# Kernel optimization log

Hardware: AMD Instinct MI355X
Metric: run time of the kernel (lower is better)

The kernel has to match this reference:

```python
import jax, jax.numpy as jnp
import numpy as np

B = 1; C = 96; NH = 4; HD = 24; WIN = 3; LL = 27; SR = 8
Dd, Hh, Ww = 16, 40, 40
N = Dd * Hh * Ww
pH, pW, pD = Hh // SR, Ww // SR, Dd // SR
PL = pH * pW * pD
T = 4096


def _build_mask():
    p = WIN // 2
    m = np.zeros((Dd + 2 * p, Hh + 2 * p, Ww + 2 * p), bool)
    m[p:Dd + p, p:Hh + p, p:Ww + p] = True
    pats = np.stack([m[dz:dz + Dd, dy:dy + Hh, dx:dx + Ww]
                     for dz in range(WIN) for dy in range(WIN) for dx in range(WIN)], axis=-1)
    return jnp.asarray(~pats.reshape(N, LL))  # True where padded (masked)

MASK = _build_mask()


def _layernorm(x, w, b, eps=1e-5):
    mu = jnp.mean(x, axis=-1, keepdims=True)
    var = jnp.var(x, axis=-1, keepdims=True)
    return (x - mu) / jnp.sqrt(var + eps) * w + b


def _l2(x, eps=1e-12):
    n = jnp.sqrt(jnp.sum(x * x, axis=-1, keepdims=True))
    return x / jnp.maximum(n, eps)


def _unfold3d(x):
    # x: (B,C,D,H,W) -> (B,C,N,27), kernel order (kd,kh,kw) as torch unfold(2).unfold(3).unfold(4)
    p = WIN // 2
    xp = jnp.pad(x, ((0, 0), (0, 0), (p, p), (p, p), (p, p)))
    pats = [xp[:, :, dz:dz + Dd, dy:dy + Hh, dx:dx + Ww]
            for dz in range(WIN) for dy in range(WIN) for dx in range(WIN)]
    return jnp.stack(pats, axis=-1).reshape(x.shape[0], C, N, LL)


def _conv3(x, w):
    return jax.lax.conv_general_dilated(x, w, (1, 1, 1), 'SAME',
                                        dimension_numbers=('NCDHW', 'OIDHW', 'NCDHW'))


def _bn(x, p, eps=1e-5):
    sh = (1, C, 1, 1, 1)
    return (x - p[2].reshape(sh)) / jnp.sqrt(p[3].reshape(sh) + eps) * p[0].reshape(sh) + p[1].reshape(sh)


def _lrelu(x):
    return jnp.where(x >= 0, x, 0.01 * x)


def _resblock(x, w1, p1, w2, p2):
    h = _lrelu(_bn(_conv3(x, w1), p1))
    h = _bn(_conv3(h, w2), p2)
    return _lrelu(h + x)


def _forward(x, relative_pos_index, relative_coords_table, seq_length_scale,
             norm_w, norm_b, gamma, w_qkvv, temperature, temperature2, query_embedding,
             rel_bias_local, learnable_tokens, learnable_bias, sr_w, sr_b,
             epa_norm_w, epa_norm_b, w_kv, cpb1_w, cpb1_b, cpb2_w, cpb2_b,
             out1_w, out1_b, out2_w, out2_b,
             c51a_w, c51a_bn, c51b_w, c51b_bn, c52a_w, c52a_bn, c52b_w, c52b_bn,
             conv8_w, conv8_b):
    Bq = x.shape[0]
    # flatten (D,H,W) -> N tokens; pos_embed=True adds 1.0 (faithful to `x + True`)
    xt = x.reshape(Bq, C, N).transpose(0, 2, 1) + 1.0
    xn = _layernorm(xt, norm_w, norm_b)
    qkvv = (xn @ w_qkvv.T).reshape(Bq, N, 4, NH, HD).transpose(2, 0, 3, 1, 4)
    q, k, v_ca, v_sa = qkvv[0], qkvv[1], qkvv[2], qkvv[3]  # (B,NH,N,HD)
    qn = _l2(q)
    qs = (qn + query_embedding) * (jax.nn.softplus(temperature) * seq_length_scale)
    k_img = k.transpose(0, 1, 3, 2).reshape(Bq, C, Dd, Hh, Ww)
    v_img = v_sa.transpose(0, 1, 3, 2).reshape(Bq, C, Dd, Hh, Ww)
    k_loc = _unfold3d(k_img).reshape(Bq, NH, HD, N, LL).transpose(0, 1, 3, 2, 4)  # (B,NH,N,HD,LL)
    v_loc = _unfold3d(v_img).reshape(Bq, NH, HD, N, LL).transpose(0, 1, 3, 2, 4)
    a_loc = jnp.einsum('bhnd,bhndk->bhnk', qs, k_loc) + rel_bias_local[:, None, :]
    a_loc = jnp.where(MASK[None, None], -jnp.inf, a_loc)
    # pooled branch (note faithful (H,W,D) reshape as in source)
    xp = xn.transpose(0, 2, 1).reshape(Bq, C, Hh, Ww, Dd)
    xp = jax.nn.gelu(jnp.einsum('oc,bcxyz->boxyz', sr_w, xp)
                     + sr_b[None, :, None, None, None], approximate=False)
    xp = xp.reshape(Bq, C, pH, SR, pW, SR, pD, SR).mean(axis=(3, 5, 7))  # adaptive avg pool
    xp = xp.reshape(Bq, C, PL).transpose(0, 2, 1)
    xp = _layernorm(xp, epa_norm_w, epa_norm_b)
    kv = (xp @ w_kv.T).reshape(Bq, PL, 2 * NH, HD).transpose(0, 2, 1, 3)
    k_pool, v_pool = kv[:, :NH], kv[:, NH:]
    tab = jax.nn.relu(relative_coords_table @ cpb1_w.T + cpb1_b) @ cpb2_w.T + cpb2_b  # (T,NH)
    pool_bias = jnp.take(tab.T, relative_pos_index.reshape(-1), axis=1).reshape(NH, N, PL)
    a_pool = jnp.einsum('bhnd,bhpd->bhnp', qs, _l2(k_pool)) + pool_bias[None]
    attn = jax.nn.softmax(jnp.concatenate([a_loc, a_pool], axis=-1), axis=-1)
    a_loc, a_pool = attn[..., :LL], attn[..., LL:]
    a_loc = jnp.einsum('bhnd,hdk->bhnk', qn, learnable_tokens) + learnable_bias[None] + a_loc
    x_loc = jnp.einsum('bhnk,bhndk->bhnd', a_loc, v_loc)
    x_pool = jnp.einsum('bhnp,bhpd->bhnd', a_pool, v_pool)
    x_sa = (x_loc + x_pool).transpose(0, 2, 1, 3).reshape(Bq, N, C)
    # channel attention branch
    qt = _l2(q.transpose(0, 1, 3, 2))
    kt = _l2(k.transpose(0, 1, 3, 2))
    vt = v_ca.transpose(0, 1, 3, 2)
    a_ca = jax.nn.softmax(jnp.einsum('bhdn,bhen->bhde', qt, kt) * temperature2, axis=-1)
    x_ca = jnp.einsum('bhde,bhen->bhdn', a_ca, vt).transpose(0, 3, 1, 2).reshape(Bq, N, C)
    epa = jnp.concatenate([x_sa @ out1_w.T + out1_b, x_ca @ out2_w.T + out2_b], axis=-1)
    ax = xt + gamma * epa
    skip = ax.reshape(Bq, Hh, Ww, Dd, C).transpose(0, 4, 1, 2, 3)  # (B,C,H,W,D)
    h = _resblock(skip, c51a_w, c51a_bn, c51b_w, c51b_bn)
    h = _resblock(h, c52a_w, c52a_bn, c52b_w, c52b_bn)
    return skip + jnp.einsum('oc,bcxyz->boxyz', conv8_w, h) + conv8_b[None, :, None, None, None]


def setup_inputs():
    key = jax.random.key(0)
    ks = iter(jax.random.split(key, 64))
    r = lambda shape, s=0.02: jax.random.normal(next(ks), shape, jnp.float32) * s
    d = {}
    d['x'] = jax.random.normal(next(ks), (B, C, Dd, Hh, Ww), jnp.float32)
    d['relative_pos_index'] = jax.random.randint(next(ks), (N * PL,), 0, T, jnp.int32)
    d['relative_coords_table'] = jax.random.normal(next(ks), (T, 3), jnp.float32)
    d['seq_length_scale'] = jnp.ones((1,), jnp.float32)
    d['norm_w'] = 1.0 + r((C,)); d['norm_b'] = r((C,))
    d['gamma'] = jnp.full((C,), 0.01, jnp.float32)
    d['w_qkvv'] = r((4 * C, C))
    d['temperature'] = jnp.full((NH, 1, 1), float(np.log(np.exp(1 / 0.24) - 1)), jnp.float32)
    d['temperature2'] = jnp.ones((NH, 1, 1), jnp.float32)
    d['query_embedding'] = r((NH, 1, HD))
    d['rel_bias_local'] = r((NH, LL), 0.0004)
    d['learnable_tokens'] = r((NH, HD, LL))
    d['learnable_bias'] = jnp.zeros((NH, 1, LL), jnp.float32)
    d['sr_w'] = r((C, C)); d['sr_b'] = r((C,))
    d['epa_norm_w'] = 1.0 + r((C,)); d['epa_norm_b'] = r((C,))
    d['w_kv'] = r((2 * C, C))
    d['cpb1_w'] = r((512, 3)); d['cpb1_b'] = r((512,))
    d['cpb2_w'] = r((NH, 512)); d['cpb2_b'] = r((NH,))
    d['out1_w'] = r((C // 2, C)); d['out1_b'] = r((C // 2,))
    d['out2_w'] = r((C // 2, C)); d['out2_b'] = r((C // 2,))
    bn = lambda: jnp.stack([1.0 + r((C,)), r((C,)), jnp.zeros((C,), jnp.float32), jnp.ones((C,), jnp.float32)])
    d['c51a_w'] = r((C, C, 3, 3, 3)); d['c51a_bn'] = bn()
    d['c51b_w'] = r((C, C, 3, 3, 3)); d['c51b_bn'] = bn()
    d['c52a_w'] = r((C, C, 3, 3, 3)); d['c52a_bn'] = bn()
    d['c52b_w'] = r((C, C, 3, 3, 3)); d['c52b_bn'] = bn()
    d['conv8_w'] = r((C, C)); d['conv8_b'] = r((C,))
    return d


def reference(x, relative_pos_index, relative_coords_table, seq_length_scale,
              norm_w, norm_b, gamma, w_qkvv, temperature, temperature2, query_embedding,
              rel_bias_local, learnable_tokens, learnable_bias, sr_w, sr_b,
              epa_norm_w, epa_norm_b, w_kv, cpb1_w, cpb1_b, cpb2_w, cpb2_b,
              out1_w, out1_b, out2_w, out2_b,
              c51a_w, c51a_bn, c51b_w, c51b_bn, c52a_w, c52a_bn, c52b_w, c52b_bn,
              conv8_w, conv8_b):
    return _forward(x, relative_pos_index, relative_coords_table, seq_length_scale,
                    norm_w, norm_b, gamma, w_qkvv, temperature, temperature2, query_embedding,
                    rel_bias_local, learnable_tokens, learnable_bias, sr_w, sr_b,
                    epa_norm_w, epa_norm_b, w_kv, cpb1_w, cpb1_b, cpb2_w, cpb2_b,
                    out1_w, out1_b, out2_w, out2_b,
                    c51a_w, c51a_bn, c51b_w, c51b_bn, c52a_w, c52a_bn, c52b_w, c52b_bn,
                    conv8_w, conv8_b)
```

## Files before the change

### kernel.cpp

```cpp
#include <hip/hip_runtime.h>
#include <hip/hip_bf16.h>

#define NN 25600
#define CC 96
#define NHh 4
#define HDd 24
#define SSLOT 2457600
#define WP 269568

typedef unsigned short ushort_t;
typedef float f32x4 __attribute__((ext_vector_type(4)));
typedef short s16x8 __attribute__((ext_vector_type(8)));
typedef _Float16 f16;
typedef f16 h2v __attribute__((ext_vector_type(2)));

__device__ __forceinline__ float LD(const void* p, int i){
  return ((const float*)p)[i];
}
__device__ __forceinline__ float b2f(ushort_t u){ return __uint_as_float(((unsigned)u)<<16); }
__device__ __forceinline__ ushort_t f2b(float f){
  unsigned u = __float_as_uint(f);
  unsigned r = (u + 0x7fffu + ((u>>16)&1u))>>16;
  return (ushort_t)r;
}
__device__ __forceinline__ ushort_t f2h(float f){
  f16 hv = (f16)f;
  return *reinterpret_cast<ushort_t*>(&hv);
}
__device__ __forceinline__ float fdot2(h2v a, h2v b, float c){
#if __has_builtin(__builtin_amdgcn_fdot2)
  return __builtin_amdgcn_fdot2(a, b, c, false);
#else
  return c + (float)a[0]*(float)b[0] + (float)a[1]*(float)b[1];
#endif
}
__device__ __forceinline__ void gl_lds16(const void* g, const void* l){
  __builtin_amdgcn_global_load_lds(
      (const __attribute__((address_space(1))) unsigned*)g,
      (__attribute__((address_space(3))) unsigned*)l, 16, 0, 0);
}

#define NEGINF (-3.0e38f)

__global__ __launch_bounds__(256) void k_ln2(
    const void* __restrict__ x, const void* __restrict__ nw,
    const void* __restrict__ nb, ushort_t* __restrict__ XNH){
  __shared__ float reds[4][64], redss[4][64];
  __shared__ ushort_t OUT[64][100];
  int tid = threadIdx.x, nl = tid&63, cg = tid>>6;
  int n = blockIdx.x*64 + nl;
  float v[24]; float s=0.f, ss=0.f;
  #pragma unroll
  for(int i=0;i<24;i++){
    float t = LD(x, (cg*24+i)*NN + n) + 1.0f;
    v[i]=t; s+=t; ss+=t*t;
  }
  reds[cg][nl]=s; redss[cg][nl]=ss;
  __syncthreads();
  float S  = reds[0][nl]+reds[1][nl]+reds[2][nl]+reds[3][nl];
  float SS = redss[0][nl]+redss[1][nl]+redss[2][nl]+redss[3][nl];
  float mu = S*(1.0f/CC);
  float inv = rsqrtf(SS*(1.0f/CC) - mu*mu + 1e-5f);
  #pragma unroll
  for(int i=0;i<24;i++){
    int c = cg*24+i;
    OUT[nl][c] = f2b((v[i]-mu)*inv*LD(nw,c) + LD(nb,c));
  }
  __syncthreads();
  for(int f=tid; f<3072; f+=256){
    int r = f/48, dp = f%48;
    unsigned pk = (unsigned)OUT[r][dp*2] | ((unsigned)OUT[r][dp*2+1]<<16);
    *reinterpret_cast<unsigned*>(XNH + (size_t)(blockIdx.x*64+r)*96 + dp*2) = pk;
  }
}

__global__ void k_prepall(
    const void* w0, const void* w1, const void* w2, const void* w3,
    const void* wq, const void* wsr, const void* w8,
    const void* o1w, const void* o1b, const void* o2w, const void* o2b,
    const void* b0, const void* b1, const void* b2, const void* b3,
    const void* ltok,
    ushort_t* __restrict__ WB2, ushort_t* __restrict__ WQH,
    ushort_t* __restrict__ WSH, ushort_t* __restrict__ W8H,
    ushort_t* __restrict__ WE, float* __restrict__ EB,
    float* __restrict__ BNS, ushort_t* __restrict__ LTOKT,
    float* __restrict__ ZB){
  int e = blockIdx.x*256 + threadIdx.x;
  if(e < 4*WP){
    int t = e/WP, r = e%WP;
    int tap = r/9984, r2 = r%9984, o = r2/104, p = r2%104;
    const void* w = (t==0)? w0 : (t==1)? w1 : (t==2)? w2 : w3;
    WB2[e] = (p<96)? f2b(LD(w, (o*96+p)*27 + tap)) : (ushort_t)0;
  }
  if(e < 36864) WQH[e] = f2b(LD(wq,e));
  if(e < 9216){ WSH[e] = f2b(LD(wsr,e)); W8H[e] = f2b(LD(w8,e)); }
  if(e < 96*192){
    int o = e/192, c2 = e%192;
    float v = 0.f;
    if(o < 48 && c2 < 96)        v = LD(o1w, o*96 + c2);
    else if(o >= 48 && c2 >= 96) v = LD(o2w, (o-48)*96 + (c2-96));
    WE[e] = f2b(v);
    if(c2 == 0) EB[o] = (o<48)? LD(o1b,o) : LD(o2b,o-48);
  }
  if(e < 384){
    int t = e/96, o = e%96;
    const void* bn = (t==0)? b0 : (t==1)? b1 : (t==2)? b2 : b3;
    float g=LD(bn,o), b=LD(bn,96+o), mu=LD(bn,192+o), var=LD(bn,288+o);
    float s = g*rsqrtf(var+1e-5f);
    BNS[t*192+o] = s;
    BNS[t*192+96+o] = b - mu*s;
  }
  if(e < 4096){
    int h = e/1024, r = e%1024, kk = r/32, d = r%32;
    float v = (d<24 && kk<27)? LD(ltok, (h*24+d)*27 + kk) : 0.f;
    LTOKT[e] = f2b(v);
  }
  if(e < 8) ZB[e] = 0.f;
}

__global__ __launch_bounds__(256) void k_rpit2(const int* __restrict__ rpi,
                                               int* __restrict__ rpiT){
  __shared__ int T[50][65];
  int n0 = blockIdx.x*64;
  int tid = threadIdx.x;
  for(int f=tid; f<3200; f+=256){
    int nl = f/50, p = f%50;
    T[p][nl] = rpi[n0*50 + f];
  }
  __syncthreads();
  for(int f=tid; f<3200; f+=256){
    int p = f>>6, nl = f&63;
    rpiT[(size_t)p*NN + n0 + nl] = T[p][nl];
  }
}

__global__ __launch_bounds__(256,2) void k_qkvsr(
    const ushort_t* __restrict__ XNH, const ushort_t* __restrict__ WQH,
    const ushort_t* __restrict__ WSH, const void* __restrict__ srb,
    float* __restrict__ out, ushort_t* __restrict__ KH,
    ushort_t* __restrict__ VH, float* __restrict__ XP2){
  int tid=threadIdx.x, w=tid>>6, lane=tid&63, lan=lane&15, grp=lane>>4;
  int n = blockIdx.x*64 + w*16 + lan;
  const ushort_t* bp = XNH + n*96;
  if(blockIdx.y < 2){
    int ybase = blockIdx.y*192;
    f32x4 acc[12];
    #pragma unroll
    for(int mt=0;mt<12;mt++) acc[mt] = (f32x4)(0.f);
    #pragma unroll
    for(int s=0;s<3;s++){
      s16x8 b = *reinterpret_cast<const s16x8*>(bp + s*32 + grp*8);
      #pragma unroll
      for(int mt=0;mt<12;mt++){
        s16x8 a = *reinterpret_cast<const s16x8*>(WQH + (ybase+mt*16+lan)*96 + s*32 + grp*8);
        acc[mt] = __builtin_amdgcn_mfma_f32_16x16x32_bf16(a, b, acc[mt], 0,0,0);
      }
    }
    #pragma unroll
    for(int mt=0;mt<12;mt++){
      int o0 = ybase + mt*16 + grp*4;
      int sl = o0/96, rr = o0%96, h = rr/24, dd = rr%24;
      f32x4 v = acc[mt];
      if(sl == 3){
        ushort4 pk = { f2h(v[0]), f2h(v[1]), f2h(v[2]), f2h(v[3]) };
        *reinterpret_cast<ushort4*>(VH + ((size_t)h*NN+n)*24 + dd) = pk;
      } else {
        *reinterpret_cast<float4*>(out + sl*SSLOT + ((size_t)h*NN+n)*24 + dd) =
            (float4){v[0],v[1],v[2],v[3]};
        if(sl == 1){
          ushort4 pk = { f2h(v[0]), f2h(v[1]), f2h(v[2]), f2h(v[3]) };
          *reinterpret_cast<ushort4*>(KH + ((size_t)h*NN+n)*24 + dd) = pk;
        }
      }
    }
  } else {
    f32x4 acc[6];
    #pragma unroll
    for(int mt=0;mt<6;mt++) acc[mt] = (f32x4)(0.f);
    #pragma unroll
    for(int s=0;s<3;s++){
      s16x8 b = *reinterpret_cast<const s16x8*>(bp + s*32 + grp*8);
      #pragma unroll
      for(int mt=0;mt<6;mt++){
        s16x8 a = *reinterpret_cast<const s16x8*>(WSH + (mt*16+lan)*96 + s*32 + grp*8);
        acc[mt] = __builtin_amdgcn_mfma_f32_16x16x32_bf16(a, b, acc[mt], 0,0,0);
      }
    }
    #pragma unroll
    for(int mt=0;mt<6;mt++){
      #pragma unroll
      for(int r=0;r<4;r++){
        int o = mt*16 + grp*4 + r;
        float y = acc[mt][r] + LD(srb,o);
        y = 0.5f*y*(1.0f + erff(y*0.70710678118f));
        XP2[o*NN+n] = y;
      }
    }
  }
}

__global__ void k_qs2(const float* __restrict__ Q, const void* __restrict__ temp,
                      const void* __restrict__ sls, const void* __restrict__ qe,
                      ushort_t* __restrict__ QNH, float* __restrict__ QS){
  int id = blockIdx.x*256 + threadIdx.x;
  if(id >= NHh*NN) return;
  int h = id/NN, n = id%NN;
  const float* qr = Q + ((size_t)h*NN+n)*24;
  float qv[24]; float ss=0.f;
  #pragma unroll
  for(int d=0;d<24;d++){ qv[d]=qr[d]; ss+=qv[d]*qv[d]; }
  float inv = 1.0f/fmaxf(sqrtf(ss), 1e-12f);
  float t = LD(temp,h);
  float sp = log1pf(expf(t)) * LD(sls,0);
  ushort_t* qo = QNH + ((size_t)h*NN+n)*32;
  float* qs = QS + ((size_t)h*NN+n)*24;
  #pragma unroll
  for(int d=0;d<24;d+=2){
    float q0 = qv[d]*inv, q1 = qv[d+1]*inv;
    unsigned pk = (unsigned)f2b(q0) | ((unsigned)f2b(q1)<<16);
    *reinterpret_cast<unsigned*>(qo + d) = pk;
    qs[d]   = (q0 + LD(qe, h*24+d))*sp;
    qs[d+1] = (q1 + LD(qe, h*24+d+1))*sp;
  }
  *reinterpret_cast<unsigned*>(qo+24)=0; *reinterpret_cast<unsigned*>(qo+26)=0;
  *reinterpret_cast<unsigned*>(qo+28)=0; *reinterpret_cast<unsigned*>(qo+30)=0;
}

__global__ __launch_bounds__(256) void k_ltm(
    const ushort_t* __restrict__ QNH, const ushort_t* __restrict__ LTOKT,
    const void* __restrict__ lbias, ushort_t* __restrict__ LTH){
  int tid=threadIdx.x, h=tid>>6, lane=tid&63, lan=lane&15, grp=lane>>4;
  int n0 = blockIdx.x*64;
  f32x4 acc[4][2];
  #pragma unroll
  for(int j=0;j<4;j++)
    #pragma unroll
    for(int t=0;t<2;t++) acc[j][t] = (f32x4)(0.f);
  #pragma unroll
  for(int j=0;j<4;j++){
    int n = n0 + j*16 + lan;
    s16x8 b = *reinterpret_cast<const s16x8*>(QNH + ((size_t)h*NN+n)*32 + grp*8);
    #pragma unroll
    for(int t=0;t<2;t++){
      s16x8 a = *reinterpret_cast<const s16x8*>(LTOKT + h*1024 + (t*16+lan)*32 + grp*8);
      acc[j][t] = __builtin_amdgcn_mfma_f32_16x16x32_bf16(a, b, acc[j][t], 0,0,0);
    }
  }
  #pragma unroll
  for(int j=0;j<4;j++){
    int n = n0 + j*16 + lan;
    #pragma unroll
    for(int t=0;t<2;t++){
      int k0 = t*16 + grp*4;
      if(k0 < 28){
        ushort4 pk;
        ushort_t* pp = reinterpret_cast<ushort_t*>(&pk);
        #pragma unroll
        for(int r=0;r<4;r++){
          int k = k0+r;
          float v = acc[j][t][r] + ((k<27)? LD(lbias, h*27+k) : 0.f);
          pp[r] = f2h(v);
        }
        *reinterpret_cast<ushort4*>(LTH + ((size_t)h*NN+n)*28 + k0) = pk;
      }
    }
  }
}

__global__ void k_pool(const float* __restrict__ XP2, float* __restrict__ pooled){
  int bb = blockIdx.x;
  int c = bb % CC, p = bb / CC;
  int ph = p/10, pw = (p%10)/2, pd = p%2;
  float s = 0.f;
  for(int t=threadIdx.x; t<512; t+=64){
    int i=t>>6, j=(t>>3)&7, k=t&7;
    int m = (ph*8+i)*640 + (pw*8+j)*16 + (pd*8+k);
    s += XP2[c*NN+m];
  }
  #pragma unroll
  for(int off=32;off;off>>=1) s += __shfl_down(s, off);
  if(threadIdx.x==0) pooled[p*CC+c] = s*(1.0f/512.0f);
}

__global__ void k_lnkv(const float* __restrict__ pooled, const void* __restrict__ ew,
                       const void* __restrict__ eb, const void* __restrict__ wkv,
                       float* __restrict__ KP, ushort_t* __restrict__ VPH){
  __shared__ float row[96], lnr[96], st[2];
  int p = blockIdx.x, t = threadIdx.x;
  if(t<96) row[t] = pooled[p*96+t];
  __syncthreads();
  if(t==0){
    float s=0.f, ss=0.f;
    for(int c=0;c<96;c++){ float v=row[c]; s+=v; ss+=v*v; }
    float mu=s*(1.0f/96.0f);
    float var=ss*(1.0f/96.0f)-mu*mu;
    st[0]=mu; st[1]=rsqrtf(var+1e-5f);
  }
  __syncthreads();
  if(t<96) lnr[t] = (row[t]-st[0])*st[1]*LD(ew,t) + LD(eb,t);
  __syncthreads();
  if(t<192){
    float a=0.f;
    for(int c=0;c<96;c++) a += LD(wkv, t*96+c)*lnr[c];
    int g=t/24, d=t%24;
    if(g<4) KP[(g*50+p)*24+d]=a;
    else    VPH[((g-4)*50+p)*24+d] = f2h(a);
  }
}

__global__ void k_kpn(const float* __restrict__ KP, ushort_t* __restrict__ KPNH){
  int t = threadIdx.x;
  if(t>=200) return;
  const float* r = KP + t*24;
  float ss=0.f;
  #pragma unroll
  for(int d=0;d<24;d++) ss += r[d]*r[d];
  float inv = 1.0f/fmaxf(sqrtf(ss),1e-12f);
  #pragma unroll
  for(int d=0;d<24;d++) KPNH[t*24+d] = f2h(r[d]*inv);
}

__global__ void k_tab(const void* __restrict__ rct, const void* __restrict__ w1,
                      const void* __restrict__ b1, const void* __restrict__ w2,
                      const void* __restrict__ b2, float* __restrict__ TAB){
  __shared__ float red[32];
  int tt = blockIdx.x, j = threadIdx.x;
  float r0=LD(rct,tt*3), r1=LD(rct,tt*3+1), r2=LD(rct,tt*3+2);
  float hj = r0*LD(w1,j*3) + r1*LD(w1,j*3+1) + r2*LD(w1,j*3+2) + LD(b1,j);
  hj = fmaxf(hj, 0.f);
  int lane=j&63, wid=j>>6;
  for(int h=0;h<4;h++){
    float v = hj*LD(w2, h*512+j);
    #pragma unroll
    for(int off=32;off;off>>=1) v += __shfl_down(v, off);
    if(lane==0) red[wid*4+h]=v;
  }
  __syncthreads();
  if(j<4){
    float s=0.f;
    for(int w=0;w<8;w++) s += red[w*4+j];
    TAB[tt*4+j] = s + LD(b2,j);
  }
}

__global__ __launch_bounds__(512) void k_attn6(
    const float* __restrict__ QS, const ushort_t* __restrict__ KH,
    const ushort_t* __restrict__ VH,
    const ushort_t* __restrict__ KPNH, const ushort_t* __restrict__ VPH,
    const float* __restrict__ TAB, const int* __restrict__ rpiT,
    const void* __restrict__ rbl, const ushort_t* __restrict__ LTH,
    ushort_t* __restrict__ XH)
{
  __shared__ ushort_t KVH[2][600*26];
  int tile = blockIdx.x, h = blockIdx.y;
  int g = tile/25, sp = tile%25, hg = sp/5, wg = sp%5;
  int tid = threadIdx.x;
  int role = tid>>8, q = tid & 255;
  int wq = q>>6, l = q&63;
  int hy = l>>3, wx = l&7;
  int d0 = g*4 + wq;
  int h0 = hg*8+hy, w0 = wg*8+wx;
  int n = d0*1600 + h0*40 + w0;

  const ushort_t* KHh = KH + (size_t)h*NN*24;
  const ushort_t* VHh = VH + (size_t)h*NN*24;
  for(int f=tid; f<3600; f+=512){
    int t = f/1800, rem = f%1800, row = rem/3, qq = rem%3;
    int dr = row/100, yr = (row%100)/10, xr = row%10;
    int zc = min(max(g*4+dr-1,0),15), yc = min(max(hg*8+yr-1,0),39), xc = min(max(wg*8+xr-1,0),39);
    const ushort_t* src = (t? VHh : KHh) + (size_t)(zc*1600+yc*40+xc)*24 + qq*8;
    const unsigned* s32 = reinterpret_cast<const unsigned*>(src);
    unsigned a0=s32[0], a1=s32[1], a2=s32[2], a3=s32[3];
    unsigned* d32 = reinterpret_cast<unsigned*>(&KVH[t][row*26 + qq*8]);
    d32[0]=a0; d32[1]=a1; d32[2]=a2; d32[3]=a3;
  }

  h2v qp[12];
  {
    const float* qsp = QS + ((size_t)h*NN+n)*24;
    #pragma unroll
    for(int d=0; d<24; d+=4){
      float4 a = *reinterpret_cast<const float4*>(qsp+d);
      qp[d/2]   = (h2v){ (f16)a.x, (f16)a.y };
      qp[d/2+1] = (h2v){ (f16)a.z, (f16)a.w };
    }
  }
  __syncthreads();

  float m_r, s_r;
  h2v accA[12], accT[12];
  #pragma unroll
  for(int j=0;j<12;j++){ accA[j]=(h2v){(f16)0.f,(f16)0.f}; accT[j]=(h2v){(f16)0.f,(f16)0.f}; }

  const h2v* kph = reinterpret_cast<const h2v*>(KPNH) + (size_t)h*50*12;
  const h2v* vph = reinterpret_cast<const h2v*>(VPH)  + (size_t)h*50*12;

  if(role==0){
    float av[39]; unsigned okm=0;
    #pragma unroll
    for(int k=0;k<27;k++){
      int kz=k/9, ky=(k%9)/3, kx=k%3;
      bool ok = (unsigned)(d0+kz-1)<16u && (unsigned)(h0+ky-1)<40u && (unsigned)(w0+kx-1)<40u;
      float sc = NEGINF;
      if(ok){
        okm |= 1u<<k;
        const h2v* kr = reinterpret_cast<const h2v*>(
            &KVH[0][((wq+kz)*100 + (hy+ky)*10 + (wx+kx))*26]);
        sc = LD(rbl, h*27+k);
        #pragma unroll
        for(int j=0;j<12;j++) sc = fdot2(kr[j], qp[j], sc);
      }
      av[k]=sc;
    }
    #pragma unroll
    for(int p=0;p<12;p++){
      float sc = TAB[rpiT[(size_t)p*NN+n]*4 + h];
      const h2v* kr = kph + p*12;
      #pragma unroll
      for(int j=0;j<12;j++) sc = fdot2(kr[j], qp[j], sc);
      av[27+p]=sc;
    }
    float m = av[0];
    #pragma unroll
    for(int k=1;k<39;k++) m = fmaxf(m, av[k]);
    const f16* ltp = reinterpret_cast<const f16*>(LTH) + ((size_t)h*NN+n)*28;
    float s = 0.f;
    #pragma unroll
    for(int k=0;k<27;k++){
      if(okm>>k & 1u){
        int kz=k/9, ky=(k%9)/3, kx=k%3;
        float e = __expf(av[k]-m);
        s += e;
        float ltv = (float)ltp[k];
        h2v we = { (f16)e, (f16)e };
        h2v wt = { (f16)ltv, (f16)ltv };
        const h2v* vr = reinterpret_cast<const h2v*>(
            &KVH[1][((wq+kz)*100 + (hy+ky)*10 + (wx+kx))*26]);
        #pragma unroll
        for(int j=0;j<12;j++){
          accA[j] = vr[j]*we + accA[j];
          accT[j] = vr[j]*wt + accT[j];
        }
      }
    }
    #pragma unroll
    for(int p=0;p<12;p++){
      float e = __expf(av[27+p]-m);
      s += e;
      h2v we = { (f16)e, (f16)e };
      const h2v* vr = vph + p*12;
      #pragma unroll
      for(int j=0;j<12;j++) accA[j] = vr[j]*we + accA[j];
    }
    m_r = m; s_r = s;
  } else {
    float av[38];
    #pragma unroll
    for(int p=0;p<38;p++){
      int pp = p+12;
      float sc = TAB[rpiT[(size_t)pp*NN+n]*4 + h];
      const h2v* kr = kph + pp*12;
      #pragma unroll
      for(int j=0;j<12;j++) sc = fdot2(kr[j], qp[j], sc);
      av[p]=sc;
    }
    float m = av[0];
    #pragma unroll
    for(int p=1;p<38;p++) m = fmaxf(m, av[p]);
    float s = 0.f;
    #pragma unroll
    for(int p=0;p<38;p++){
      float e = __expf(av[p]-m);
      s += e;
      h2v we = { (f16)e, (f16)e };
      const h2v* vr = vph + (p+12)*12;
      #pragma unroll
      for(int j=0;j<12;j++) accA[j] = vr[j]*we + accA[j];
    }
    m_r = m; s_r = s;
  }
  __syncthreads();

  float* PP = (float*)&KVH[0][0];
  if(role==1){
    PP[q*15+0] = m_r;
    PP[q*15+1] = s_r;
    #pragma unroll
    for(int j=0;j<12;j++){
      h2v a = accA[j];
      PP[q*15+2+j] = __uint_as_float(*reinterpret_cast<unsigned*>(&a));
    }
  }
  __syncthreads();

  float* TRF = (float*)&KVH[0][0] + 4096;
  if(role==0){
    float mp = PP[q*15+0], sp2 = PP[q*15+1];
    float m = fmaxf(m_r, mp);
    float a = __expf(m_r - m), b = __expf(mp - m);
    float inv = 1.0f/(a*s_r + b*sp2);
    #pragma unroll
    for(int j=0;j<12;j++){
      unsigned pb = __float_as_uint(PP[q*15+2+j]);
      h2v ap = *reinterpret_cast<h2v*>(&pb);
      float v0 = (a*(float)accA[j][0] + b*(float)ap[0])*inv + (float)accT[j][0];
      float v1 = (a*(float)accA[j][1] + b*(float)ap[1])*inv + (float)accT[j][1];
      TRF[q*25 + 2*j]   = v0;
      TRF[q*25 + 2*j+1] = v1;
    }
  }
  __syncthreads();

  for(int f=tid; f<3072; f+=512){
    int q2 = f/12, dp = f%12;
    int w2 = q2>>6, l2 = q2&63;
    int n2 = (g*4+w2)*1600 + (hg*8+(l2>>3))*40 + (wg*8+(l2&7));
    float v0 = TRF[q2*25+dp*2], v1 = TRF[q2*25+dp*2+1];
    unsigned pk = (unsigned)f2b(v0) | ((unsigned)f2b(v1)<<16);
    *reinterpret_cast<unsigned*>(XH + (size_t)n2*192 + h*24 + dp*2) = pk;
  }
}

__global__ void k_cascore2(const float* __restrict__ Q, const float* __restrict__ K,
                           float* __restrict__ PAR){
  __shared__ float red[4][26];
  int hd = blockIdx.x, h = hd/24, d = hd%24;
  int n0 = blockIdx.y*3200;
  float acc[24]; float qss=0.f, kss=0.f;
  #pragma unroll
  for(int e=0;e<24;e++) acc[e]=0.f;
  for(int i=threadIdx.x; i<3200; i+=256){
    int n = n0 + i;
    const float4* kr4 = reinterpret_cast<const float4*>(K + ((size_t)h*NN+n)*24);
    float4 k0=kr4[0], k1=kr4[1], k2=kr4[2], k3=kr4[3], k4=kr4[4], k5=kr4[5];
    float qv = Q[((size_t)h*NN+n)*24+d];
    qss += qv*qv;
    float kd = LD(K, ((size_t)h*NN+n)*24+d);
    kss += kd*kd;
    acc[0]+=qv*k0.x; acc[1]+=qv*k0.y; acc[2]+=qv*k0.z; acc[3]+=qv*k0.w;
    acc[4]+=qv*k1.x; acc[5]+=qv*k1.y; acc[6]+=qv*k1.z; acc[7]+=qv*k1.w;
    acc[8]+=qv*k2.x; acc[9]+=qv*k2.y; acc[10]+=qv*k2.z; acc[11]+=qv*k2.w;
    acc[12]+=qv*k3.x; acc[13]+=qv*k3.y; acc[14]+=qv*k3.z; acc[15]+=qv*k3.w;
    acc[16]+=qv*k4.x; acc[17]+=qv*k4.y; acc[18]+=qv*k4.z; acc[19]+=qv*k4.w;
    acc[20]+=qv*k5.x; acc[21]+=qv*k5.y; acc[22]+=qv*k5.z; acc[23]+=qv*k5.w;
  }
  int lane=threadIdx.x&63, wid=threadIdx.x>>6;
  #pragma unroll
  for(int j=0;j<26;j++){
    float v = (j<24)? acc[j] : (j==24? qss : kss);
    #pragma unroll
    for(int off=32;off;off>>=1) v += __shfl_down(v, off);
    if(lane==0) red[wid][j]=v;
  }
  __syncthreads();
  if(threadIdx.x<26){
    int j=threadIdx.x;
    PAR[((size_t)blockIdx.y*96+hd)*26 + j] = red[0][j]+red[1][j]+red[2][j]+red[3][j];
  }
}

__global__ void k_casm2(const float* __restrict__ PAR, const void* __restrict__ t2,
                        float* __restrict__ ACA){
  __shared__ float kinv_s[96];
  int t = threadIdx.x;
  int h = t/24;
  float S[24]; float qss=0.f, kss=0.f;
  #pragma unroll
  for(int e=0;e<24;e++) S[e]=0.f;
  for(int c=0;c<8;c++){
    const float* pp = PAR + ((size_t)c*96+t)*26;
    #pragma unroll
    for(int e=0;e<24;e++) S[e] += pp[e];
    qss += pp[24]; kss += pp[25];
  }
  float qi = 1.0f/fmaxf(sqrtf(qss),1e-12f);
  kinv_s[t] = 1.0f/fmaxf(sqrtf(kss),1e-12f);
  __syncthreads();
  float tv = LD(t2,h);
  float v[24]; float m = NEGINF;
  #pragma unroll
  for(int e=0;e<24;e++){
    v[e] = S[e]*qi*kinv_s[h*24+e]*tv;
    m = fmaxf(m, v[e]);
  }
  float s=0.f;
  #pragma unroll
  for(int e=0;e<24;e++){ v[e]=__expf(v[e]-m); s+=v[e]; }
  float inv=1.0f/s;
  #pragma unroll
  for(int e=0;e<24;e++) ACA[t*24+e] = v[e]*inv;
}

__global__ void k_caout2(const float* __restrict__ ACA, const float* __restrict__ VCA,
                         ushort_t* __restrict__ XH){
  __shared__ float A[2304];
  int t = threadIdx.x;
  for(int f=t; f<2304; f+=256) A[f] = ACA[f];
  __syncthreads();
  int h = t>>6, l = t&63;
  int n = blockIdx.x*64 + l;
  float vr[24];
  const float* vp = VCA + ((size_t)h*NN+n)*24;
  #pragma unroll
  for(int e=0;e<24;e+=4){
    float4 v = *reinterpret_cast<const float4*>(vp+e);
    vr[e]=v.x; vr[e+1]=v.y; vr[e+2]=v.z; vr[e+3]=v.w;
  }
  float o[24];
  #pragma unroll
  for(int d=0;d<24;d++){
    float a=0.f;
    const float* ar = A + (h*24+d)*24;
    #pragma unroll
    for(int e=0;e<24;e++) a += ar[e]*vr[e];
    o[d]=a;
  }
  #pragma unroll
  for(int d=0;d<24;d+=2){
    unsigned pk = (unsigned)f2b(o[d]) | ((unsigned)f2b(o[d+1])<<16);
    *reinterpret_cast<unsigned*>(XH + (size_t)n*192 + 96 + h*24 + d) = pk;
  }
}

__global__ __launch_bounds__(256,2) void k_epam(
    const ushort_t* __restrict__ XH, const ushort_t* __restrict__ WE,
    const float* __restrict__ EB, const void* __restrict__ x,
    const void* __restrict__ gamma,
    float* __restrict__ SKIPF, ushort_t* __restrict__ SKIPH){
  int tid=threadIdx.x, w=tid>>6, lane=tid&63, lan=lane&15, grp=lane>>4;
  int n = blockIdx.x*64 + w*16 + lan;
  const ushort_t* bp = XH + (size_t)n*192;
  f32x4 acc[6];
  #pragma unroll
  for(int mt=0;mt<6;mt++) acc[mt] = (f32x4)(0.f);
  #pragma unroll
  for(int s=0;s<6;s++){
    s16x8 b = *reinterpret_cast<const s16x8*>(bp + s*32 + grp*8);
    #pragma unroll
    for(int mt=0;mt<6;mt++){
      s16x8 a = *reinterpret_cast<const s16x8*>(WE + (mt*16+lan)*192 + s*32 + grp*8);
      acc[mt] = __builtin_amdgcn_mfma_f32_16x16x32_bf16(a, b, acc[mt], 0,0,0);
    }
  }
  #pragma unroll
  for(int mt=0;mt<6;mt++){
    #pragma unroll
    for(int r=0;r<4;r++){
      int o = mt*16 + grp*4 + r;
      float e = acc[mt][r] + EB[o];
      float v = LD(x, o*NN+n) + 1.0f + LD(gamma,o)*e;
      SKIPF[(size_t)n*96+o] = v;
      SKIPH[(size_t)n*96+o] = f2b(v);
    }
  }
}

__global__ __launch_bounds__(256,2) void k_convm8(
    const ushort_t* __restrict__ IN, const ushort_t* __restrict__ WB2,
    const float* __restrict__ BNS, const float* __restrict__ resf,
    const float* __restrict__ ZB,
    ushort_t* __restrict__ outh, float* __restrict__ outf)
{
  __shared__ ushort_t BUF[2][16640];
  int tid = threadIdx.x;
  int w = tid>>6, lane = tid&63;
  int lan = lane&15, grp = lane>>4;
  int bs = (blockIdx.x&7)*50 + (blockIdx.x>>3);
  int n0 = bs*64;

  auto STAGE = [&](int tap, ushort_t* buf){
    int dx=tap/9-1, dy=(tap%9)/3-1, dz=tap%3-1;
    int off = dx*640 + dy*16 + dz;
    const ushort_t* wsrc = WB2 + tap*9984;
    #pragma unroll
    for(int i=0;i<9;i++){
      int cb = i*256 + w*64;
      if(cb >= 2080) break;
      int c = cb + lane;
      const void* src;
      if(c < 1248){
        src = wsrc + c*8;
      } else {
        int c2 = c - 1248;
        int r = c2/13, p = c2%13;
        int nn = n0 + r;
        int X = nn/640, rr2 = nn%640, Y = rr2/16, Z = nn&15;
        bool ok = (p<12) && (unsigned)(X+dx)<40u && (unsigned)(Y+dy)<40u && (unsigned)(Z+dz)<16u;
        src = ok ? (const void*)(IN + (size_t)(nn+off)*96 + p*8) : (const void*)ZB;
      }
      if(c < 2080) gl_lds16(src, buf + cb*8);
    }
  };

  f32x4 acc[6];
  #pragma unroll
  for(int mt=0;mt<6;mt++) acc[mt] = (f32x4)(0.f);

  STAGE(0, BUF[0]);
  asm volatile("s_waitcnt vmcnt(0)" ::: "memory");
  __builtin_amdgcn_s_barrier();

  for(int tap=0; tap<27; ++tap){
    if(tap<26){
      STAGE(tap+1, BUF[(tap+1)&1]);
      asm volatile("s_waitcnt vmcnt(8)" ::: "memory");
    } else {
      asm volatile("s_waitcnt vmcnt(0)" ::: "memory");
    }
    __builtin_amdgcn_s_barrier();
    __builtin_amdgcn_sched_barrier(0);
    const ushort_t* Ab = BUF[tap&1];
    const ushort_t* Bb = Ab + 9984;
    s16x8 bfr[3];
    #pragma unroll
    for(int s=0;s<3;s++)
      bfr[s] = *reinterpret_cast<const s16x8*>(Bb + (w*16+lan)*104 + s*32 + grp*8);
    #pragma unroll
    for(int mt=0;mt<6;mt++){
      #pragma unroll
      for(int s=0;s<3;s++){
        s16x8 a = *reinterpret_cast<const s16x8*>(Ab + (mt*16+lan)*104 + s*32 + grp*8);
        acc[mt] = __builtin_amdgcn_mfma_f32_16x16x32_bf16(a, bfr[s], acc[mt], 0,0,0);
      }
    }
    __builtin_amdgcn_s_barrier();
  }

  float* TR = (float*)&BUF[0][0];
  int nl = w*16 + lan;
  #pragma unroll
  for(int mt=0;mt<6;mt++){
    int ob = mt*16 + grp*4;
    float4 vv;
    vv.x = acc[mt][0]*BNS[ob+0] + BNS[96+ob+0];
    vv.y = acc[mt][1]*BNS[ob+1] + BNS[96+ob+1];
    vv.z = acc[mt][2]*BNS[ob+2] + BNS[96+ob+2];
    vv.w = acc[mt][3]*BNS[ob+3] + BNS[96+ob+3];
    *reinterpret_cast<float4*>(TR + nl*100 + ob) = vv;
  }
  __syncthreads();
  for(int f=tid; f<3072; f+=256){
    int r = f/48, cp = f%48;
    int n = n0 + r;
    float v0 = TR[r*100+cp*2], v1 = TR[r*100+cp*2+1];
    if(resf){ v0 += resf[(size_t)n*96+cp*2]; v1 += resf[(size_t)n*96+cp*2+1]; }
    v0 = (v0>=0.f)? v0 : 0.01f*v0;
    v1 = (v1>=0.f)? v1 : 0.01f*v1;
    unsigned pk = (unsigned)f2b(v0) | ((unsigned)f2b(v1)<<16);
    *reinterpret_cast<unsigned*>(outh + (size_t)n*96 + cp*2) = pk;
    if(outf){
      float2 fo; fo.x=v0; fo.y=v1;
      *reinterpret_cast<float2*>(outf + (size_t)n*96 + cp*2) = fo;
    }
  }
}

__global__ __launch_bounds__(256,2) void k_finm(
    const float* __restrict__ SKIPF, const ushort_t* __restrict__ T3H,
    const ushort_t* __restrict__ W8H, const void* __restrict__ b,
    float* __restrict__ out){
  int tid=threadIdx.x, w=tid>>6, lane=tid&63, lan=lane&15, grp=lane>>4;
  int n = blockIdx.x*64 + w*16 + lan;
  const ushort_t* bp = T3H + n*96;
  f32x4 acc[6];
  #pragma unroll
  for(int mt=0;mt<6;mt++) acc[mt] = (f32x4)(0.f);
  #pragma unroll
  for(int s=0;s<3;s++){
    s16x8 bb = *reinterpret_cast<const s16x8*>(bp + s*32 + grp*8);
    #pragma unroll
    for(int mt=0;mt<6;mt++){
      s16x8 a = *reinterpret_cast<const s16x8*>(W8H + (mt*16+lan)*96 + s*32 + grp*8);
      acc[mt] = __builtin_amdgcn_mfma_f32_16x16x32_bf16(a, bb, acc[mt], 0,0,0);
    }
  }
  #pragma unroll
  for(int mt=0;mt<6;mt++){
    #pragma unroll
    for(int r=0;r<4;r++){
      int o = mt*16 + grp*4 + r;
      out[o*NN+n] = SKIPF[(size_t)n*96+o] + acc[mt][r] + LD(b,o);
    }
  }
}

extern "C" void kernel_launch(void* const* d_in, const int* in_sizes, int n_in,
                              void* d_out, int out_size, void* d_ws, size_t ws_size,
                              hipStream_t stream){
  const void* x     = d_in[0];
  const int*  rpi   = (const int*)d_in[1];
  const void* rct   = d_in[2];
  const void* sls   = d_in[3];
  const void* nw    = d_in[4];
  const void* nb    = d_in[5];
  const void* gamma = d_in[6];
  const void* wqkvv = d_in[7];
  const void* temp  = d_in[8];
  const void* temp2 = d_in[9];
  const void* qe    = d_in[10];
  const void* rbl   = d_in[11];
  const void* ltok  = d_in[12];
  const void* lbias = d_in[13];
  const void* srw   = d_in[14];
  const void* srb   = d_in[15];
  const void* epaw  = d_in[16];
  const void* epab  = d_in[17];
  const void* wkv   = d_in[18];
  const void* c1w   = d_in[19];
  const void* c1b   = d_in[20];
  const void* c2w   = d_in[21];
  const void* c2b   = d_in[22];
  const void* o1w   = d_in[23];
  const void* o1b   = d_in[24];
  const void* o2w   = d_in[25];
  const void* o2b   = d_in[26];
  const void* w51a  = d_in[27];
  const void* bn51a = d_in[28];
  const void* w51b  = d_in[29];
  const void* bn51b = d_in[30];
  const void* w52a  = d_in[31];
  const void* bn52a = d_in[32];
  const void* w52b  = d_in[33];
  const void* bn52b = d_in[34];
  const void* w8    = d_in[35];
  const void* b8    = d_in[36];

  float* ws = (float*)d_ws;
  const size_t S = SSLOT;
  ushort_t* XNH = (ushort_t*)ws;
  float* SKIPF = ws;
  float* Q     = ws + 1*S;
  float* Kb    = ws + 2*S;
  float* T2F   = ws + 2*S;
  float* VCA   = ws + 3*S;
  ushort_t* KH = (ushort_t*)(ws + 4*S);
  ushort_t* VH = KH + SSLOT;
  ushort_t* QNH = (ushort_t*)(ws + 5*S);
  float* QS    = ws + 6*S;
  ushort_t* XH = (ushort_t*)(ws + 7*S);
  int*   rpiT  = (int*)(ws + 8*S);
  float* XP2   = ws + 7*S;
  ushort_t* SKIPH = (ushort_t*)(ws + 4*S);
  ushort_t* T1H   = SKIPH + SSLOT;
  ushort_t* T2H   = (ushort_t*)(ws + 5*S);
  ushort_t* T3H   = T2H + SSLOT;
  float* SM  = ws + 9*S;
  float* pooled = SM;
  float* KP     = SM + 4800;
  float* TAB    = SM + 19200;
  float* ACA    = SM + 38080;
  ushort_t* WB2 = (ushort_t*)(SM + 40960);
  float* BNS    = SM + 40960 + 539136;
  ushort_t* WQH = (ushort_t*)(BNS + 768);
  ushort_t* WSH = WQH + 36864;
  ushort_t* W8H = WSH + 9216;
  ushort_t* WE  = W8H + 9216;
  float* EB     = BNS + 768 + 18432 + 4608 + 4608 + 9216;
  float* PAR    = EB + 96;
  ushort_t* KPNH = (ushort_t*)(PAR + 19968);
  ushort_t* VPH  = KPNH + 4800;
  ushort_t* LTOKT= VPH + 4800;
  ushort_t* LTH  = LTOKT + 4096;
  float* ZB      = (float*)(LTH + 2867200);

  k_prepall<<<4212, 256, 0, stream>>>(w51a, w51b, w52a, w52b, wqkvv, srw, w8,
                                      o1w, o1b, o2w, o2b,
                                      bn51a, bn51b, bn52a, bn52b, ltok,
                                      WB2, WQH, WSH, W8H, WE, EB, BNS, LTOKT, ZB);
  k_rpit2 <<<400,   256, 0, stream>>>(rpi, rpiT);
  k_ln2   <<<400,   256, 0, stream>>>(x, nw, nb, XNH);
  k_qkvsr <<<dim3(400,3), 256, 0, stream>>>(XNH, WQH, WSH, srb, Q, KH, VH, XP2);
  k_qs2   <<<400,   256, 0, stream>>>(Q, temp, sls, qe, QNH, QS);
  k_ltm   <<<400,   256, 0, stream>>>(QNH, LTOKT, lbias, LTH);
  k_pool  <<<4800,  64,  0, stream>>>(XP2, pooled);
  k_lnkv  <<<50,    256, 0, stream>>>(pooled, epaw, epab, wkv, KP, VPH);
  k_kpn   <<<1,     256, 0, stream>>>(KP, KPNH);
  k_tab   <<<4096,  512, 0, stream>>>(rct, c1w, c1b, c2w, c2b, TAB);
  k_attn6 <<<dim3(100,4), 512, 0, stream>>>(QS, KH, VH, KPNH, VPH, TAB, rpiT,
                                            rbl, LTH, XH);
  k_cascore2<<<dim3(96,8), 256, 0, stream>>>(Q, Kb, PAR);
  k_casm2 <<<1,     96,  0, stream>>>(PAR, temp2, ACA);
  k_caout2<<<400,   256, 0, stream>>>(ACA, VCA, XH);
  k_epam  <<<400,   256, 0, stream>>>(XH, WE, EB, x, gamma, SKIPF, SKIPH);
  k_convm8<<<400, 256, 0, stream>>>(SKIPH, WB2,        BNS,     nullptr, ZB, T1H, nullptr);
  k_convm8<<<400, 256, 0, stream>>>(T1H,   WB2+WP,     BNS+192, SKIPF,   ZB, T2H, T2F);
  k_convm8<<<400, 256, 0, stream>>>(T2H,   WB2+2*WP,   BNS+384, nullptr, ZB, T1H, nullptr);
  k_convm8<<<400, 256, 0, stream>>>(T1H,   WB2+3*WP,   BNS+576, T2F,     ZB, T3H, nullptr);
  k_finm  <<<400, 256, 0, stream>>>(SKIPF, T3H, W8H, b8, (float*)d_out);
}
```

Measured before the change: 331.6 us.

## Merge prep, rpi transpose, layernorm and CPB table into one launch; fuse qnorm with LTM

Four independent setup kernels (weight prep, relative-position-index transpose, input layernorm, CPB bias table) are merged into a single launch that dispatches on block index. The CPB table part now uses 256 threads that each handle two hidden units instead of 512 threads. The query-normalise kernel is also fused with the learnable-token matmul, so normalised queries are staged in LDS rather than written to and re-read from global memory. This cuts launch count and one global round trip, at the cost of a larger heterogeneous kernel whose register use and LDS size are set by its largest branch.

Result: faster. 312.2 us (-5.9%).

```diff
diff --git a/kernel.cpp b/kernel.cpp
--- a/kernel.cpp
+++ b/kernel.cpp
@@ -42,95 +42,121 @@
 
 #define NEGINF (-3.0e38f)
 
-__global__ __launch_bounds__(256) void k_ln2(
-    const void* __restrict__ x, const void* __restrict__ nw,
-    const void* __restrict__ nb, ushort_t* __restrict__ XNH){
-  __shared__ float reds[4][64], redss[4][64];
-  __shared__ ushort_t OUT[64][100];
-  int tid = threadIdx.x, nl = tid&63, cg = tid>>6;
-  int n = blockIdx.x*64 + nl;
-  float v[24]; float s=0.f, ss=0.f;
-  #pragma unroll
-  for(int i=0;i<24;i++){
-    float t = LD(x, (cg*24+i)*NN + n) + 1.0f;
-    v[i]=t; s+=t; ss+=t*t;
-  }
-  reds[cg][nl]=s; redss[cg][nl]=ss;
-  __syncthreads();
-  float S  = reds[0][nl]+reds[1][nl]+reds[2][nl]+reds[3][nl];
-  float SS = redss[0][nl]+redss[1][nl]+redss[2][nl]+redss[3][nl];
-  float mu = S*(1.0f/CC);
-  float inv = rsqrtf(SS*(1.0f/CC) - mu*mu + 1e-5f);
-  #pragma unroll
-  for(int i=0;i<24;i++){
-    int c = cg*24+i;
-    OUT[nl][c] = f2b((v[i]-mu)*inv*LD(nw,c) + LD(nb,c));
-  }
-  __syncthreads();
-  for(int f=tid; f<3072; f+=256){
-    int r = f/48, dp = f%48;
-    unsigned pk = (unsigned)OUT[r][dp*2] | ((unsigned)OUT[r][dp*2+1]<<16);
-    *reinterpret_cast<unsigned*>(XNH + (size_t)(blockIdx.x*64+r)*96 + dp*2) = pk;
-  }
-}
-
-__global__ void k_prepall(
+__global__ __launch_bounds__(256) void k_mega(
     const void* w0, const void* w1, const void* w2, const void* w3,
     const void* wq, const void* wsr, const void* w8,
     const void* o1w, const void* o1b, const void* o2w, const void* o2b,
-    const void* b0, const void* b1, const void* b2, const void* b3,
+    const void* b0, const void* b1, const void* b2bn, const void* b3,
     const void* ltok,
     ushort_t* __restrict__ WB2, ushort_t* __restrict__ WQH,
     ushort_t* __restrict__ WSH, ushort_t* __restrict__ W8H,
     ushort_t* __restrict__ WE, float* __restrict__ EB,
     float* __restrict__ BNS, ushort_t* __restrict__ LTOKT,
-    float* __restrict__ ZB){
-  int e = blockIdx.x*256 + threadIdx.x;
-  if(e < 4*WP){
-    int t = e/WP, r = e%WP;
-    int tap = r/9984, r2 = r%9984, o = r2/104, p = r2%104;
-    const void* w = (t==0)? w0 : (t==1)? w1 : (t==2)? w2 : w3;
-    WB2[e] = (p<96)? f2b(LD(w, (o*96+p)*27 + tap)) : (ushort_t)0;
-  }
-  if(e < 36864) WQH[e] = f2b(LD(wq,e));
-  if(e < 9216){ WSH[e] = f2b(LD(wsr,e)); W8H[e] = f2b(LD(w8,e)); }
-  if(e < 96*192){
-    int o = e/192, c2 = e%192;
-    float v = 0.f;
-    if(o < 48 && c2 < 96)        v = LD(o1w, o*96 + c2);
-    else if(o >= 48 && c2 >= 96) v = LD(o2w, (o-48)*96 + (c2-96));
-    WE[e] = f2b(v);
-    if(c2 == 0) EB[o] = (o<48)? LD(o1b,o) : LD(o2b,o-48);
-  }
-  if(e < 384){
-    int t = e/96, o = e%96;
-    const void* bn = (t==0)? b0 : (t==1)? b1 : (t==2)? b2 : b3;
-    float g=LD(bn,o), b=LD(bn,96+o), mu=LD(bn,192+o), var=LD(bn,288+o);
-    float s = g*rsqrtf(var+1e-5f);
-    BNS[t*192+o] = s;
-    BNS[t*192+96+o] = b - mu*s;
-  }
-  if(e < 4096){
-    int h = e/1024, r = e%1024, kk = r/32, d = r%32;
-    float v = (d<24 && kk<27)? LD(ltok, (h*24+d)*27 + kk) : 0.f;
-    LTOKT[e] = f2b(v);
-  }
-  if(e < 8) ZB[e] = 0.f;
-}
-
-__global__ __launch_bounds__(256) void k_rpit2(const int* __restrict__ rpi,
-                                               int* __restrict__ rpiT){
-  __shared__ int T[50][65];
-  int n0 = blockIdx.x*64;
-  int tid = threadIdx.x;
-  for(int f=tid; f<3200; f+=256){
-    int nl = f/50, p = f%50;
-    T[p][nl] = rpi[n0*50 + f];
-  }
-  __syncthreads();
-  for(int f=tid; f<3200; f+=256){
-    int p = f>>6, nl = f&63;
-    rpiT[(size_t)p*NN + n0 + nl] = T[p][nl];
+    float* __restrict__ ZB,
+    const int* __restrict__ rpi, int* __restrict__ rpiT,
+    const void* __restrict__ x, const void* __restrict__ nw,
+    const void* __restrict__ nb, ushort_t* __restrict__ XNH,
+    const void* __restrict__ rct, const void* __restrict__ w1t,
+    const void* __restrict__ b1t, const void* __restrict__ w2t,
+    const void* __restrict__ b2t, float* __restrict__ TAB)
+{
+  __shared__ __align__(16) char SMEM[15400];
+  int b = blockIdx.x, tid = threadIdx.x;
+  if(b < 4212){
+    int e = b*256 + tid;
+    {
+      int t = e/WP, r = e%WP;
+      int tap = r/9984, r2 = r%9984, o = r2/104, p = r2%104;
+      const void* w = (t==0)? w0 : (t==1)? w1 : (t==2)? w2 : w3;
+      WB2[e] = (p<96)? f2b(LD(w, (o*96+p)*27 + tap)) : (ushort_t)0;
+    }
+    if(e < 36864) WQH[e] = f2b(LD(wq,e));
+    if(e < 9216){ WSH[e] = f2b(LD(wsr,e)); W8H[e] = f2b(LD(w8,e)); }
+    if(e < 96*192){
+      int o = e/192, c2 = e%192;
+      float v = 0.f;
+      if(o < 48 && c2 < 96)        v = LD(o1w, o*96 + c2);
+      else if(o >= 48 && c2 >= 96) v = LD(o2w, (o-48)*96 + (c2-96));
+      WE[e] = f2b(v);
+      if(c2 == 0) EB[o] = (o<48)? LD(o1b,o) : LD(o2b,o-48);
+    }
+    if(e < 384){
+      int t = e/96, o = e%96;
+      const void* bn = (t==0)? b0 : (t==1)? b1 : (t==2)? b2bn : b3;
+      float g=LD(bn,o), bb=LD(bn,96+o), mu=LD(bn,192+o), var=LD(bn,288+o);
+      float s = g*rsqrtf(var+1e-5f);
+      BNS[t*192+o] = s;
+      BNS[t*192+96+o] = bb - mu*s;
+    }
+    if(e < 4096){
+      int h = e/1024, r = e%1024, kk = r/32, d = r%32;
+      float v = (d<24 && kk<27)? LD(ltok, (h*24+d)*27 + kk) : 0.f;
+      LTOKT[e] = f2b(v);
+    }
+    if(e < 8) ZB[e] = 0.f;
+  } else if(b < 4612){
+    int* T = (int*)SMEM;
+    int n0 = (b-4212)*64;
+    for(int f=tid; f<3200; f+=256){
+      int nl = f/50, p = f%50;
+      T[p*65+nl] = rpi[n0*50 + f];
+    }
+    __syncthreads();
+    for(int f=tid; f<3200; f+=256){
+      int p = f>>6, nl = f&63;
+      rpiT[(size_t)p*NN + n0 + nl] = T[p*65+nl];
+    }
+  } else if(b < 5012){
+    float* reds  = (float*)SMEM;
+    float* redss = reds + 256;
+    ushort_t* OUT = (ushort_t*)(redss + 256);
+    int bx = b - 4612;
+    int nl = tid&63, cg = tid>>6;
+    int n = bx*64 + nl;
+    float v[24]; float s=0.f, ss=0.f;
+    #pragma unroll
+    for(int i=0;i<24;i++){
+      float t = LD(x, (cg*24+i)*NN + n) + 1.0f;
+      v[i]=t; s+=t; ss+=t*t;
+    }
+    reds[cg*64+nl]=s; redss[cg*64+nl]=ss;
+    __syncthreads();
+    float S  = reds[nl]+reds[64+nl]+reds[128+nl]+reds[192+nl];
+    float SS = redss[nl]+redss[64+nl]+redss[128+nl]+redss[192+nl];
+    float mu = S*(1.0f/CC);
+    float inv = rsqrtf(SS*(1.0f/CC) - mu*mu + 1e-5f);
+    #pragma unroll
+    for(int i=0;i<24;i++){
+      int c = cg*24+i;
+      OUT[nl*100+c] = f2b((v[i]-mu)*inv*LD(nw,c) + LD(nb,c));
+    }
+    __syncthreads();
+    for(int f=tid; f<3072; f+=256){
+      int r = f/48, dp = f%48;
+      unsigned pk = (unsigned)OUT[r*100+dp*2] | ((unsigned)OUT[r*100+dp*2+1]<<16);
+      *reinterpret_cast<unsigned*>(XNH + (size_t)(bx*64+r)*96 + dp*2) = pk;
+    }
+  } else {
+    float* red = (float*)SMEM;
+    int tt = b - 5012, j = tid;
+    float r0=LD(rct,tt*3), r1=LD(rct,tt*3+1), r2=LD(rct,tt*3+2);
+    float hA = r0*LD(w1t,j*3) + r1*LD(w1t,j*3+1) + r2*LD(w1t,j*3+2) + LD(b1t,j);
+    hA = fmaxf(hA, 0.f);
+    int j2 = j + 256;
+    float hB = r0*LD(w1t,j2*3) + r1*LD(w1t,j2*3+1) + r2*LD(w1t,j2*3+2) + LD(b1t,j2);
+    hB = fmaxf(hB, 0.f);
+    int lane=j&63, wid=j>>6;
+    for(int h=0;h<4;h++){
+      float v = hA*LD(w2t, h*512+j) + hB*LD(w2t, h*512+j2);
+      #pragma unroll
+      for(int off=32;off;off>>=1) v += __shfl_down(v, off);
+      if(lane==0) red[wid*4+h]=v;
+    }
+    __syncthreads();
+    if(j<4){
+      float s = red[j] + red[4+j] + red[8+j] + red[12+j];
+      TAB[tt*4+j] = s + LD(b2t,j);
+    }
   }
 }
 
@@ -199,69 +225,67 @@
   }
 }
 
-__global__ void k_qs2(const float* __restrict__ Q, const void* __restrict__ temp,
-                      const void* __restrict__ sls, const void* __restrict__ qe,
-                      ushort_t* __restrict__ QNH, float* __restrict__ QS){
-  int id = blockIdx.x*256 + threadIdx.x;
-  if(id >= NHh*NN) return;
-  int h = id/NN, n = id%NN;
+__global__ __launch_bounds__(256) void k_qsltm(
+    const float* __restrict__ Q, const void* __restrict__ temp,
+    const void* __restrict__ sls, const void* __restrict__ qe,
+    const ushort_t* __restrict__ LTOKT, const void* __restrict__ lbias,
+    float* __restrict__ QS, ushort_t* __restrict__ LTH){
+  __shared__ ushort_t QL[4][64][32];
+  int tid = threadIdx.x;
+  int h = tid>>6, nl = tid&63;
+  int n0 = blockIdx.x*64, n = n0 + nl;
   const float* qr = Q + ((size_t)h*NN+n)*24;
-  float qv[24]; float ss=0.f;
-  #pragma unroll
-  for(int d=0;d<24;d++){ qv[d]=qr[d]; ss+=qv[d]*qv[d]; }
-  float inv = 1.0f/fmaxf(sqrtf(ss), 1e-12f);
+  float qv[24]; float ssum=0.f;
+  #pragma unroll
+  for(int d=0;d<24;d++){ qv[d]=qr[d]; ssum+=qv[d]*qv[d]; }
+  float inv = 1.0f/fmaxf(sqrtf(ssum), 1e-12f);
   float t = LD(temp,h);
   float sp = log1pf(expf(t)) * LD(sls,0);
-  ushort_t* qo = QNH + ((size_t)h*NN+n)*32;
   float* qs = QS + ((size_t)h*NN+n)*24;
   #pragma unroll
   for(int d=0;d<24;d+=2){
     float q0 = qv[d]*inv, q1 = qv[d+1]*inv;
     unsigned pk = (unsigned)f2b(q0) | ((unsigned)f2b(q1)<<16);
-    *reinterpret_cast<unsigned*>(qo + d) = pk;
+    *reinterpret_cast<unsigned*>(&QL[h][nl][d]) = pk;
     qs[d]   = (q0 + LD(qe, h*24+d))*sp;
     qs[d+1] = (q1 + LD(qe, h*24+d+1))*sp;
   }
-  *reinterpret_cast<unsigned*>(qo+24)=0; *reinterpret_cast<unsigned*>(qo+26)=0;
-  *reinterpret_cast<unsigned*>(qo+28)=0; *reinterpret_cast<unsigned*>(qo+30)=0;
-}
-
-__global__ __launch_bounds__(256) void k_ltm(
-    const ushort_t* __restrict__ QNH, const ushort_t* __restrict__ LTOKT,
-    const void* __restrict__ lbias, ushort_t* __restrict__ LTH){
-  int tid=threadIdx.x, h=tid>>6, lane=tid&63, lan=lane&15, grp=lane>>4;
-  int n0 = blockIdx.x*64;
+  *reinterpret_cast<unsigned*>(&QL[h][nl][24]) = 0;
+  *reinterpret_cast<unsigned*>(&QL[h][nl][26]) = 0;
+  *reinterpret_cast<unsigned*>(&QL[h][nl][28]) = 0;
+  *reinterpret_cast<unsigned*>(&QL[h][nl][30]) = 0;
+  __syncthreads();
+  int lane=tid&63, lan=lane&15, grp=lane>>4;
   f32x4 acc[4][2];
   #pragma unroll
   for(int j=0;j<4;j++)
     #pragma unroll
-    for(int t=0;t<2;t++) acc[j][t] = (f32x4)(0.f);
+    for(int tt=0;tt<2;tt++) acc[j][tt] = (f32x4)(0.f);
   #pragma unroll
   for(int j=0;j<4;j++){
-    int n = n0 + j*16 + lan;
-    s16x8 b = *reinterpret_cast<const s16x8*>(QNH + ((size_t)h*NN+n)*32 + grp*8);
-    #pragma unroll
-    for(int t=0;t<2;t++){
-      s16x8 a = *reinterpret_cast<const s16x8*>(LTOKT + h*1024 + (t*16+lan)*32 + grp*8);
-      acc[j][t] = __builtin_amdgcn_mfma_f32_16x16x32_bf16(a, b, acc[j][t], 0,0,0);
+    s16x8 b = *reinterpret_cast<const s16x8*>(&QL[h][j*16+lan][grp*8]);
+    #pragma unroll
+    for(int tt=0;tt<2;tt++){
+      s16x8 a = *reinterpret_cast<const s16x8*>(LTOKT + h*1024 + (tt*16+lan)*32 + grp*8);
+      acc[j][tt] = __builtin_amdgcn_mfma_f32_16x16x32_bf16(a, b, acc[j][tt], 0,0,0);
     }
   }
   #pragma unroll
   for(int j=0;j<4;j++){
-    int n = n0 + j*16 + lan;
-    #pragma unroll
-    for(int t=0;t<2;t++){
-      int k0 = t*16 + grp*4;
+    int nn = n0 + j*16 + lan;
+    #pragma unroll
+    for(int tt=0;tt<2;tt++){
+      int k0 = tt*16 + grp*4;
       if(k0 < 28){
         ushort4 pk;
         ushort_t* pp = reinterpret_cast<ushort_t*>(&pk);
         #pragma unroll
         for(int r=0;r<4;r++){
           int k = k0+r;
-          float v = acc[j][t][r] + ((k<27)? LD(lbias, h*27+k) : 0.f);
+          float v = acc[j][tt][r] + ((k<27)? LD(lbias, h*27+k) : 0.f);
           pp[r] = f2h(v);
         }
-        *reinterpret_cast<ushort4*>(LTH + ((size_t)h*NN+n)*28 + k0) = pk;
+        *reinterpret_cast<ushort4*>(LTH + ((size_t)h*NN+nn)*28 + k0) = pk;
       }
     }
   }
@@ -318,29 +342,6 @@
   float inv = 1.0f/fmaxf(sqrtf(ss),1e-12f);
   #pragma unroll
   for(int d=0;d<24;d++) KPNH[t*24+d] = f2h(r[d]*inv);
-}
-
-__global__ void k_tab(const void* __restrict__ rct, const void* __restrict__ w1,
-                      const void* __restrict__ b1, const void* __restrict__ w2,
-                      const void* __restrict__ b2, float* __restrict__ TAB){
-  __shared__ float red[32];
-  int tt = blockIdx.x, j = threadIdx.x;
-  float r0=LD(rct,tt*3), r1=LD(rct,tt*3+1), r2=LD(rct,tt*3+2);
-  float hj = r0*LD(w1,j*3) + r1*LD(w1,j*3+1) + r2*LD(w1,j*3+2) + LD(b1,j);
-  hj = fmaxf(hj, 0.f);
-  int lane=j&63, wid=j>>6;
-  for(int h=0;h<4;h++){
-    float v = hj*LD(w2, h*512+j);
-    #pragma unroll
-    for(int off=32;off;off>>=1) v += __shfl_down(v, off);
-    if(lane==0) red[wid*4+h]=v;
-  }
-  __syncthreads();
-  if(j<4){
-    float s=0.f;
-    for(int w=0;w<8;w++) s += red[w*4+j];
-    TAB[tt*4+j] = s + LD(b2,j);
-  }
 }
 
 __global__ __launch_bounds__(512) void k_attn6(
@@ -835,7 +836,6 @@
   float* VCA   = ws + 3*S;
   ushort_t* KH = (ushort_t*)(ws + 4*S);
   ushort_t* VH = KH + SSLOT;
-  ushort_t* QNH = (ushort_t*)(ws + 5*S);
   float* QS    = ws + 6*S;
   ushort_t* XH = (ushort_t*)(ws + 7*S);
   int*   rpiT  = (int*)(ws + 8*S);
@@ -863,19 +863,18 @@
   ushort_t* LTH  = LTOKT + 4096;
   float* ZB      = (float*)(LTH + 2867200);
 
-  k_prepall<<<4212, 256, 0, stream>>>(w51a, w51b, w52a, w52b, wqkvv, srw, w8,
-                                      o1w, o1b, o2w, o2b,
-                                      bn51a, bn51b, bn52a, bn52b, ltok,
-                                      WB2, WQH, WSH, W8H, WE, EB, BNS, LTOKT, ZB);
-  k_rpit2 <<<400,   256, 0, stream>>>(rpi, rpiT);
-  k_ln2   <<<400,   256, 0, stream>>>(x, nw, nb, XNH);
+  k_mega  <<<9108, 256, 0, stream>>>(w51a, w51b, w52a, w52b, wqkvv, srw, w8,
+                                     o1w, o1b, o2w, o2b,
+                                     bn51a, bn51b, bn52a, bn52b, ltok,
+                                     WB2, WQH, WSH, W8H, WE, EB, BNS, LTOKT, ZB,
+                                     rpi, rpiT,
+                                     x, nw, nb, XNH,
+                                     rct, c1w, c1b, c2w, c2b, TAB);
   k_qkvsr <<<dim3(400,3), 256, 0, stream>>>(XNH, WQH, WSH, srb, Q, KH, VH, XP2);
-  k_qs2   <<<400,   256, 0, stream>>>(Q, temp, sls, qe, QNH, QS);
-  k_ltm   <<<400,   256, 0, stream>>>(QNH, LTOKT, lbias, LTH);
+  k_qsltm <<<400,   256, 0, stream>>>(Q, temp, sls, qe, LTOKT, lbias, QS, LTH);
   k_pool  <<<4800,  64,  0, stream>>>(XP2, pooled);
   k_lnkv  <<<50,    256, 0, stream>>>(pooled, epaw, epab, wkv, KP, VPH);
   k_kpn   <<<1,     256, 0, stream>>>(KP, KPNH);
-  k_tab   <<<4096,  512, 0, stream>>>(rct, c1w, c1b, c2w, c2b, TAB);
   k_attn6 <<<dim3(100,4), 512, 0, stream>>>(QS, KH, VH, KPNH, VPH, TAB, rpiT,
                                             rbl, LTH, XH);
   k_cascore2<<<dim3(96,8), 256, 0, stream>>>(Q, Kb, PAR);
```
